# Kernel tuning notes

Hardware: AMD Instinct MI355X
Metric: run time of the kernel (lower is better)

Reference implementation:

```python
import jax, jax.numpy as jnp
import numpy as np

NUM_K = 10
T = 1.0  # softmax temperature (forward default)


def setup_inputs() -> dict:
    key = jax.random.key(0)
    k1, k2, k3, k4 = jax.random.split(key, 4)
    B, H, P, D = 64, 12, 197, 64
    return {
        "att_s": jax.random.normal(k1, (B, H, P, P), dtype=jnp.float32),
        "att_t": jax.random.normal(k2, (B, H, P, P), dtype=jnp.float32),
        "v_s": jax.random.normal(k3, (B, H, P, D), dtype=jnp.float32),
        "v_t": jax.random.normal(k4, (B, H, P, D), dtype=jnp.float32),
    }


def _topk_masked_attend(att, v):
    # att: [B,H,P,P] logits, v: [B,H,P,D]
    a = jax.nn.softmax(att / T, axis=-1)
    # kth-largest value per row acts as the threshold (torch.topk semantics)
    margin = jax.lax.top_k(a, NUM_K)[0][..., -1]           # [B,H,P]
    a = a * (a >= margin[..., None])                        # keep top-k entries
    norm = a.sum(-1)                                        # [B,H,P]
    return jnp.einsum("bhpq,bhqd->bhpd", a, v) / norm[..., None]


def reference(att_s, att_t, v_s, v_t):
    out_s = _topk_masked_attend(att_s, v_s)
    out_t = _topk_masked_attend(att_t, v_t)
    # nn.MSELoss default reduction='mean'
    return jnp.mean(jnp.square(out_s - out_t))
```

## Files before the change

### kernel.cpp

```cpp
#include <hip/hip_runtime.h>
#include <cstdint>
#include <cfloat>

#define NK 10
constexpr int Pp   = 197;
constexpr int Dd   = 64;
constexpr int ROWS = 64 * 12 * 197;
constexpr int BLK  = 128;
constexpr int WPB  = BLK / 64;
constexpr int RPW  = 64;
constexpr int RPB  = RPW * WPB;
constexpr int NBLK = ROWS / RPB;
constexpr int CH   = 32;
constexpr int NFULL = Pp / CH;
constexpr int TAIL  = Pp - NFULL * CH;
constexpr float INV_N = 1.0f / 9682944.0f;

constexpr int RPB_B = 16;
constexpr int NB_B  = ROWS / RPB_B;

__device__ __forceinline__ uint32_t fbits(float x) { return __float_as_uint(x); }
__device__ __forceinline__ float    bfl(uint32_t u) { return __uint_as_float(u); }

template <int CW>
__device__ __forceinline__ void consume_chunk(const float* __restrict__ trow,
                                              float a[NK]) {
#pragma unroll
  for (int j = 0; j < CW; ++j) {
    float x = trow[j];
#pragma unroll
    for (int s = 0; s < NK - 1; ++s) a[s] = fmaxf(a[s], fminf(x, a[s + 1]));
    a[NK - 1] = fmaxf(a[NK - 1], x);
  }
}

__device__ __forceinline__ void load_chunk_regs(const float* __restrict__ slab,
                                                int c, int l, float pf[CH]) {
  if (c < NFULL) {
    const int r0 = l >> 5, j = l & 31;
    const uint32_t col = (uint32_t)(c * CH + j);
    const float* p = slab + c * CH + r0 * Pp + j;
#pragma unroll
    for (int i = 0; i < CH; ++i) {
      float x = __builtin_nontemporal_load(&p[i * 2 * Pp]);
      pf[i] = bfl((fbits(x) & 0xFFFFFF00u) | col);
    }
  } else {
    const float* cbase = slab + NFULL * CH;
#pragma unroll
    for (int i = 0; i < TAIL; ++i) {
      int e = l + i * 64;
      int r = e / TAIL, j = e % TAIL;
      float x = __builtin_nontemporal_load(&cbase[r * Pp + j]);
      pf[i] = bfl((fbits(x) & 0xFFFFFF00u) | (uint32_t)(NFULL * CH + j));
    }
  }
}

__device__ __forceinline__ void store_chunk(float (*twv)[CH + 1], int c, int l,
                                            const float pf[CH]) {
  if (c < NFULL) {
    const int r0 = l >> 5, j = l & 31;
#pragma unroll
    for (int i = 0; i < CH; ++i) twv[r0 + 2 * i][j] = pf[i];
  } else {
#pragma unroll
    for (int i = 0; i < TAIL; ++i) {
      int e = l + i * 64;
      twv[e / TAIL][e % TAIL] = pf[i];
    }
  }
}

__global__ __launch_bounds__(BLK, 4) void select_kernel(
    const float* __restrict__ att_s, const float* __restrict__ att_t,
    float* __restrict__ wpk ) {
  __shared__ float tile[WPB][RPW][CH + 1];

  const int t = threadIdx.x;
  const int wv = t >> 6, l = t & 63;
  const int bi = blockIdx.x;
  const int tensor = (bi >= NBLK) ? 1 : 0;
  const int slab = bi - tensor * NBLK;
  const float* A = tensor ? att_t : att_s;
  const int rowbase = slab * RPB + wv * RPW;

  float a[NK];
#pragma unroll
  for (int k = 0; k < NK; ++k) a[k] = -FLT_MAX;

  const float* slabp = A + (size_t)rowbase * Pp;
  float (*twv)[CH + 1] = tile[wv];
  float pf[CH];

  load_chunk_regs(slabp, 0, l, pf);
  for (int c = 0; c <= NFULL; ++c) {
    store_chunk(twv, c, l, pf);
    if (c < NFULL) {
      load_chunk_regs(slabp, c + 1, l, pf);
      consume_chunk<CH>(twv[l], a);
    } else {
      consume_chunk<TAIL>(twv[l], a);
    }
  }

  float mx = a[NK - 1];
  float e[NK], s = 0.f;
#pragma unroll
  for (int k = 0; k < NK; ++k) { e[k] = __expf(a[k] - mx); s += e[k]; }
  float inv = 1.0f / s;

  float* flat = &twv[0][0];
#pragma unroll
  for (int k = 0; k < NK; ++k) {
    float w = e[k] * inv;
    flat[l * NK + k] = bfl((fbits(w) & 0xFFFFFF00u) | (fbits(a[k]) & 0xFFu));
  }
  float* dst = wpk + ((size_t)tensor * ROWS + rowbase) * NK;
#pragma unroll
  for (int i = 0; i < NK; ++i) dst[l + i * 64] = flat[l + i * 64];
}

__global__ __launch_bounds__(1024) void gather_kernel(
    const float* __restrict__ v_s, const float* __restrict__ v_t,
    const float* __restrict__ wpk, float* __restrict__ partial) {
  const int t = threadIdx.x, wv = t >> 6, l = t & 63;
  int row = blockIdx.x * RPB_B + wv;
  row = __builtin_amdgcn_readfirstlane(row);
  const int bh = row / Pp;
  const float* vsb = v_s + (size_t)bh * (Pp * Dd) + l;
  const float* vtb = v_t + (size_t)bh * (Pp * Dd) + l;
  const float* w0 = wpk + (size_t)row * NK;
  const float* w1 = wpk + ((size_t)ROWS + row) * NK;

  float acc = 0.f;
#pragma unroll
  for (int k = 0; k < NK; ++k) {
    float w = w0[k];
    int idx = (int)(fbits(w) & 0xFFu);
    acc = fmaf(w, vsb[idx * Dd], acc);
  }
#pragma unroll
  for (int k = 0; k < NK; ++k) {
    float w = w1[k];
    int idx = (int)(fbits(w) & 0xFFu);
    acc = fmaf(-w, vtb[idx * Dd], acc);
  }
  float sq = acc * acc;
#pragma unroll
  for (int off = 32; off > 0; off >>= 1) sq += __shfl_xor(sq, off, 64);

  __shared__ float red[RPB_B];
  if (l == 0) red[wv] = sq;
  __syncthreads();
  if (t == 0) {
    float tot = 0.f;
#pragma unroll
    for (int i = 0; i < RPB_B; ++i) tot += red[i];
    partial[blockIdx.x] = tot;
  }
}

__global__ __launch_bounds__(1024) void reduce_kernel(
    const float* __restrict__ partial, float* __restrict__ out) {
  const int t = threadIdx.x, wv = t >> 6, l = t & 63;
  float s = 0.f;
  for (int i = t; i < NB_B; i += 1024) s += partial[i];
#pragma unroll
  for (int off = 32; off > 0; off >>= 1) s += __shfl_xor(s, off, 64);
  __shared__ float red[16];
  if (l == 0) red[wv] = s;
  __syncthreads();
  if (t == 0) {
    float tot = 0.f;
#pragma unroll
    for (int i = 0; i < 16; ++i) tot += red[i];
    out[0] = tot * INV_N;
  }
}

extern "C" void kernel_launch(void* const* d_in, const int* in_sizes, int n_in,
                              void* d_out, int out_size, void* d_ws,
                              size_t ws_size, hipStream_t stream) {
  const float* att_s = (const float*)d_in[0];
  const float* att_t = (const float*)d_in[1];
  const float* v_s = (const float*)d_in[2];
  const float* v_t = (const float*)d_in[3];
  float* out = (float*)d_out;

  float* wpk = (float*)d_ws;
  float* partial = wpk + (size_t)2 * ROWS * NK;

  select_kernel<<<2 * NBLK, BLK, 0, stream>>>(att_s, att_t, wpk);
  gather_kernel<<<NB_B, 1024, 0, stream>>>(v_s, v_t, wpk, partial);
  reduce_kernel<<<1, 1024, 0, stream>>>(partial, out);
}
```

Before: 375.6 us.

## Stage per-head V tiles in LDS and gather top-k rows from shared memory

The gather kernel now uses one block per (batch, head). Each block bulk-loads the full V_s and V_t slabs into LDS with vector nontemporal loads, then each wave loops over rows and reads its top-k V rows from shared memory. This replaces scattered global reads, which re-fetched the same V rows across many blocks, with one coalesced load per head. The cost is about 100KB of LDS per block, which limits occupancy to one block per CU. The column-index packing also moves from the load step to the LDS store step in the select kernel.

```diff
diff --git a/kernel.cpp b/kernel.cpp
--- a/kernel.cpp
+++ b/kernel.cpp
@@ -5,7 +5,8 @@
 #define NK 10
 constexpr int Pp   = 197;
 constexpr int Dd   = 64;
-constexpr int ROWS = 64 * 12 * 197;
+constexpr int BH   = 64 * 12;
+constexpr int ROWS = BH * Pp;
 constexpr int BLK  = 128;
 constexpr int WPB  = BLK / 64;
 constexpr int RPW  = 64;
@@ -16,8 +17,10 @@
 constexpr int TAIL  = Pp - NFULL * CH;
 constexpr float INV_N = 1.0f / 9682944.0f;
 
-constexpr int RPB_B = 16;
-constexpr int NB_B  = ROWS / RPB_B;
+constexpr int GBLK = 1024;
+constexpr int GW   = GBLK / 64;
+
+typedef float f32x4 __attribute__((ext_vector_type(4)));
 
 __device__ __forceinline__ uint32_t fbits(float x) { return __float_as_uint(x); }
 __device__ __forceinline__ float    bfl(uint32_t u) { return __uint_as_float(u); }
@@ -38,21 +41,16 @@
                                                 int c, int l, float pf[CH]) {
   if (c < NFULL) {
     const int r0 = l >> 5, j = l & 31;
-    const uint32_t col = (uint32_t)(c * CH + j);
     const float* p = slab + c * CH + r0 * Pp + j;
 #pragma unroll
-    for (int i = 0; i < CH; ++i) {
-      float x = __builtin_nontemporal_load(&p[i * 2 * Pp]);
-      pf[i] = bfl((fbits(x) & 0xFFFFFF00u) | col);
-    }
+    for (int i = 0; i < CH; ++i)
+      pf[i] = __builtin_nontemporal_load(&p[i * 2 * Pp]);
   } else {
     const float* cbase = slab + NFULL * CH;
 #pragma unroll
     for (int i = 0; i < TAIL; ++i) {
       int e = l + i * 64;
-      int r = e / TAIL, j = e % TAIL;
-      float x = __builtin_nontemporal_load(&cbase[r * Pp + j]);
-      pf[i] = bfl((fbits(x) & 0xFFFFFF00u) | (uint32_t)(NFULL * CH + j));
+      pf[i] = __builtin_nontemporal_load(&cbase[(e / TAIL) * Pp + (e % TAIL)]);
     }
   }
 }
@@ -61,13 +59,16 @@
                                             const float pf[CH]) {
   if (c < NFULL) {
     const int r0 = l >> 5, j = l & 31;
-#pragma unroll
-    for (int i = 0; i < CH; ++i) twv[r0 + 2 * i][j] = pf[i];
+    const uint32_t col = (uint32_t)(c * CH + j);
+#pragma unroll
+    for (int i = 0; i < CH; ++i)
+      twv[r0 + 2 * i][j] = bfl((fbits(pf[i]) & 0xFFFFFF00u) | col);
   } else {
 #pragma unroll
     for (int i = 0; i < TAIL; ++i) {
       int e = l + i * 64;
-      twv[e / TAIL][e % TAIL] = pf[i];
+      uint32_t col = (uint32_t)(NFULL * CH + e % TAIL);
+      twv[e / TAIL][e % TAIL] = bfl((fbits(pf[i]) & 0xFFFFFF00u) | col);
     }
   }
 }
@@ -121,43 +122,59 @@
   for (int i = 0; i < NK; ++i) dst[l + i * 64] = flat[l + i * 64];
 }
 
-__global__ __launch_bounds__(1024) void gather_kernel(
+__global__ __launch_bounds__(GBLK) void gather_kernel(
     const float* __restrict__ v_s, const float* __restrict__ v_t,
     const float* __restrict__ wpk, float* __restrict__ partial) {
+  __shared__ float ls[2][Pp][Dd];
+  __shared__ float red[GW];
+
   const int t = threadIdx.x, wv = t >> 6, l = t & 63;
-  int row = blockIdx.x * RPB_B + wv;
-  row = __builtin_amdgcn_readfirstlane(row);
-  const int bh = row / Pp;
-  const float* vsb = v_s + (size_t)bh * (Pp * Dd) + l;
-  const float* vtb = v_t + (size_t)bh * (Pp * Dd) + l;
-  const float* w0 = wpk + (size_t)row * NK;
-  const float* w1 = wpk + ((size_t)ROWS + row) * NK;
-
-  float acc = 0.f;
-#pragma unroll
-  for (int k = 0; k < NK; ++k) {
-    float w = w0[k];
-    int idx = (int)(fbits(w) & 0xFFu);
-    acc = fmaf(w, vsb[idx * Dd], acc);
-  }
-#pragma unroll
-  for (int k = 0; k < NK; ++k) {
-    float w = w1[k];
-    int idx = (int)(fbits(w) & 0xFFu);
-    acc = fmaf(-w, vtb[idx * Dd], acc);
-  }
-  float sq = acc * acc;
-#pragma unroll
-  for (int off = 32; off > 0; off >>= 1) sq += __shfl_xor(sq, off, 64);
-
-  __shared__ float red[RPB_B];
-  if (l == 0) red[wv] = sq;
+  const int b = blockIdx.x;
+
+  constexpr int NV4 = Pp * Dd / 4;
+  const f32x4* s4 = (const f32x4*)(v_s + (size_t)b * (Pp * Dd));
+  const f32x4* t4 = (const f32x4*)(v_t + (size_t)b * (Pp * Dd));
+  f32x4* d0 = (f32x4*)&ls[0][0][0];
+  f32x4* d1 = (f32x4*)&ls[1][0][0];
+  for (int i = t; i < NV4; i += GBLK) {
+    d0[i] = __builtin_nontemporal_load(&s4[i]);
+    d1[i] = __builtin_nontemporal_load(&t4[i]);
+  }
+  __syncthreads();
+
+  const float* lsS = &ls[0][0][0];
+  const float* lsT = &ls[1][0][0];
+
+  float wsum = 0.f;
+  for (int r = wv; r < Pp; r += GW) {
+    const float* w0 = wpk + (size_t)(b * Pp + r) * NK;
+    const float* w1 = wpk + ((size_t)ROWS + b * Pp + r) * NK;
+    float acc = 0.f;
+#pragma unroll
+    for (int k = 0; k < NK; ++k) {
+      float w = w0[k];
+      int idx = (int)(fbits(w) & 0xFFu);
+      acc = fmaf(w, lsS[idx * Dd + l], acc);
+    }
+#pragma unroll
+    for (int k = 0; k < NK; ++k) {
+      float w = w1[k];
+      int idx = (int)(fbits(w) & 0xFFu);
+      acc = fmaf(-w, lsT[idx * Dd + l], acc);
+    }
+    float sq = acc * acc;
+#pragma unroll
+    for (int off = 32; off > 0; off >>= 1) sq += __shfl_xor(sq, off, 64);
+    wsum += sq;
+  }
+
+  if (l == 0) red[wv] = wsum;
   __syncthreads();
   if (t == 0) {
     float tot = 0.f;
 #pragma unroll
-    for (int i = 0; i < RPB_B; ++i) tot += red[i];
-    partial[blockIdx.x] = tot;
+    for (int i = 0; i < GW; ++i) tot += red[i];
+    partial[b] = tot;
   }
 }
 
@@ -165,7 +182,7 @@
     const float* __restrict__ partial, float* __restrict__ out) {
   const int t = threadIdx.x, wv = t >> 6, l = t & 63;
   float s = 0.f;
-  for (int i = t; i < NB_B; i += 1024) s += partial[i];
+  for (int i = t; i < BH; i += 1024) s += partial[i];
 #pragma unroll
   for (int off = 32; off > 0; off >>= 1) s += __shfl_xor(s, off, 64);
   __shared__ float red[16];
@@ -192,6 +209,6 @@
   float* partial = wpk + (size_t)2 * ROWS * NK;
 
   select_kernel<<<2 * NBLK, BLK, 0, stream>>>(att_s, att_t, wpk);
-  gather_kernel<<<NB_B, 1024, 0, stream>>>(v_s, v_t, wpk, partial);
+  gather_kernel<<<BH, GBLK, 0, stream>>>(v_s, v_t, wpk, partial);
   reduce_kernel<<<1, 1024, 0, stream>>>(partial, out);
 }
```

New measurement: 355.7 us. 5.3% less time.
